# Kernel tuning notes

Measured on AMD Instinct MI355X. Metric: run time of the kernel, lower is better.

The kernel has to match this reference:

```python
import jax, jax.numpy as jnp
import numpy as np

B, T, D, H, P, A = 128, 512, 512, 512, 512, 32  # envs, steps, feat, lstm hidden, latent, actions


def setup_inputs() -> dict:
    key = jax.random.key(0)
    ks = jax.random.split(key, 30)
    N = B * T
    lin = lambda k, o, i: 0.02 * jax.random.normal(k, (o, i), jnp.float32)
    vec = lambda k, o: 0.02 * jax.random.normal(k, (o,), jnp.float32)
    inp = {
        'features': jax.random.normal(ks[0], (N, D), jnp.float32),
        'episode_starts': (jax.random.uniform(ks[1], (N,)) < 0.02).astype(jnp.float32),
        'h0_pi': jax.random.normal(ks[2], (1, B, H), jnp.float32),
        'c0_pi': jax.random.normal(ks[3], (1, B, H), jnp.float32),
        'h0_vf': jax.random.normal(ks[4], (1, B, H), jnp.float32),
        'c0_vf': jax.random.normal(ks[5], (1, B, H), jnp.float32),
        'Wih_pi': lin(ks[6], 4 * H, D), 'Whh_pi': lin(ks[7], 4 * H, H),
        'bih_pi': vec(ks[8], 4 * H), 'bhh_pi': vec(ks[9], 4 * H),
        'Wih_vf': lin(ks[10], 4 * H, D), 'Whh_vf': lin(ks[11], 4 * H, H),
        'bih_vf': vec(ks[12], 4 * H), 'bhh_vf': vec(ks[13], 4 * H),
        'pol_w1': lin(ks[14], P, H), 'pol_b1': vec(ks[15], P),
        'pol_w2': lin(ks[16], P, P), 'pol_b2': vec(ks[17], P),
        'val_w1': lin(ks[18], P, H), 'val_b1': vec(ks[19], P),
        'val_w2': lin(ks[20], P, P), 'val_b2': vec(ks[21], P),
        'actor_w': lin(ks[22], A, P), 'actor_b': vec(ks[23], A),
        'critic_w': lin(ks[24], 1, P), 'critic_b': vec(ks[25], 1),
        'deterministic': 1,
    }
    return inp


def masked_lstm(xs, starts, h0, c0, Wih, Whh, bih, bhh):
    # xs: [T,B,D], starts: [T,B]; PyTorch gate order i,f,g,o; reset h,c where episode starts.
    def step(carry, inp):
        h, c = carry
        x, s = inp
        m = (1.0 - s)[:, None]
        h, c = h * m, c * m
        g = x @ Wih.T + bih + h @ Whh.T + bhh
        i, f, gg, o = jnp.split(g, 4, axis=-1)
        c = jax.nn.sigmoid(f) * c + jax.nn.sigmoid(i) * jnp.tanh(gg)
        h = jax.nn.sigmoid(o) * jnp.tanh(c)
        return (h, c), h
    (hT, cT), ys = jax.lax.scan(step, (h0[0], c0[0]), (xs, starts))
    return ys, hT[None], cT[None]


def mlp(x, w1, b1, w2, b2):
    return jax.nn.relu(x @ w1.T + b1) @ w2.T + b2


def reference(features, episode_starts, h0_pi, c0_pi, h0_vf, c0_vf,
              Wih_pi, Whh_pi, bih_pi, bhh_pi, Wih_vf, Whh_vf, bih_vf, bhh_vf,
              pol_w1, pol_b1, pol_w2, pol_b2, val_w1, val_b1, val_w2, val_b2,
              actor_w, actor_b, critic_w, critic_b, deterministic):
    n_seq = h0_pi.shape[1]
    d = features.shape[-1]
    xs = features.reshape(n_seq, -1, d).swapaxes(0, 1)        # [T,B,D]
    st = episode_starts.reshape(n_seq, -1).swapaxes(0, 1)     # [T,B]
    ys_pi, h_pi, c_pi = masked_lstm(xs, st, h0_pi, c0_pi, Wih_pi, Whh_pi, bih_pi, bhh_pi)
    ys_vf, h_vf, c_vf = masked_lstm(xs, st, h0_vf, c0_vf, Wih_vf, Whh_vf, bih_vf, bhh_vf)
    hsz = ys_pi.shape[-1]
    lat_pi = ys_pi.swapaxes(0, 1).reshape(-1, hsz)            # [B*T,H]
    lat_vf = ys_vf.swapaxes(0, 1).reshape(-1, hsz)
    lat_pi = mlp(lat_pi, pol_w1, pol_b1, pol_w2, pol_b2)
    lat_vf = mlp(lat_vf, val_w1, val_b1, val_w2, val_b2)
    values = lat_vf @ critic_w.T + critic_b                    # [B*T,1]
    logits = lat_pi @ actor_w.T + actor_b                      # [B*T,A]
    actions = jnp.argmax(logits, axis=-1)                      # deterministic mode
    logp = jax.nn.log_softmax(logits, axis=-1)
    log_prob = jnp.take_along_axis(logp, actions[:, None], axis=1)[:, 0]
    return actions, values, log_prob, h_pi, c_pi, h_vf, c_vf
```

## Files before the change

### kernel.cpp

```cpp
#include <hip/hip_runtime.h>
#include <math.h>

#define BB 128
#define TT 512
#define DD 512
#define HH 512
#define NN (BB*TT)
#define PP 512
#define AA 32
#define CH 64
#define CR (BB*CH)

typedef unsigned short u16;
typedef unsigned int   u32;
typedef __attribute__((ext_vector_type(8))) short short8;
typedef __attribute__((ext_vector_type(4))) float f32x4;

__device__ __forceinline__ u16 f2bf(float f){
    u32 x = __float_as_uint(f);
    u32 r = (x + 0x7fffu + ((x >> 16) & 1u)) >> 16;
    return (u16)r;
}
__device__ __forceinline__ float bf2f(u16 u){
    return __uint_as_float(((u32)u) << 16);
}
__device__ __forceinline__ f32x4 mfma16(short8 a, short8 b, f32x4 c){
    return __builtin_amdgcn_mfma_f32_16x16x32_bf16(a, b, c, 0, 0, 0);
}
__device__ __forceinline__ float sigm(float x){
    return 1.f/(1.f + __expf(-x));
}
__device__ __forceinline__ float tanh_f(float x){
    return 1.f - 2.f/(1.f + __expf(2.f*x));
}

__global__ __launch_bounds__(256) void prep_lstm_w(
    const float* __restrict__ Wih_pi, const float* __restrict__ Whh_pi,
    const float* __restrict__ bih_pi, const float* __restrict__ bhh_pi,
    const float* __restrict__ Wih_vf, const float* __restrict__ Whh_vf,
    const float* __restrict__ bih_vf, const float* __restrict__ bhh_vf,
    u16* __restrict__ wihHi, u16* __restrict__ wihLo,
    u16* __restrict__ whhHi, u16* __restrict__ whhLo,
    float* __restrict__ biasP)
{
    long i = (long)blockIdx.x*256 + threadIdx.x;
    if (i >= 2L*2048*512) return;
    int L = (int)(i >> 20);
    int rem = (int)(i & 1048575);
    int c = rem >> 9, k = rem & 511;
    int u = c >> 2, g = c & 3;
    long src = (long)(g*512 + u)*512 + k;
    float wih = (L ? Wih_vf : Wih_pi)[src];
    float whh = (L ? Whh_vf : Whh_pi)[src];
    u16 h1 = f2bf(wih); wihHi[i] = h1; wihLo[i] = f2bf(wih - bf2f(h1));
    u16 h2 = f2bf(whh); whhHi[i] = h2; whhLo[i] = f2bf(whh - bf2f(h2));
    if (k == 0) {
        float b = (L ? bih_vf : bih_pi)[g*512+u] + (L ? bhh_vf : bhh_pi)[g*512+u];
        biasP[L*2048 + c] = b;
    }
}

__global__ __launch_bounds__(256) void prep_mlp_w(
    const float* __restrict__ w1pi, const float* __restrict__ w1vf,
    const float* __restrict__ w2pi, const float* __restrict__ w2vf,
    const float* __restrict__ b1pi, const float* __restrict__ b1vf,
    const float* __restrict__ b2pi, const float* __restrict__ b2vf,
    u16* __restrict__ mHi, u16* __restrict__ mLo, float* __restrict__ biasM)
{
    long i = (long)blockIdx.x*256 + threadIdx.x;
    if (i >= 4L*262144) return;
    int mat = (int)(i >> 18);
    int rem = (int)(i & 262143);
    const float* src = mat==0 ? w1pi : mat==1 ? w1vf : mat==2 ? w2pi : w2vf;
    float v = src[rem];
    u16 h = f2bf(v); mHi[i] = h; mLo[i] = f2bf(v - bf2f(h));
    if (rem < 512) {
        const float* bs = mat==0 ? b1pi : mat==1 ? b1vf : mat==2 ? b2pi : b2vf;
        biasM[mat*512 + rem] = bs[rem];
    }
}

__global__ __launch_bounds__(256) void init_state_k(
    const float* __restrict__ h0_pi, const float* __restrict__ c0_pi,
    const float* __restrict__ h0_vf, const float* __restrict__ c0_vf,
    const float* __restrict__ starts,
    u16* __restrict__ hHi, u16* __restrict__ hLo, float* __restrict__ cT,
    float* __restrict__ startsT)
{
    int i = blockIdx.x*256 + threadIdx.x;
    if (i < NN) {
        int e = i >> 9, t = i & 511;
        startsT[t*128 + e] = starts[i];
    }
    if (i >= 2*BB*HH) return;
    int L = i >> 16; int r = i & 65535;
    int e = r >> 9, u = r & 511;
    float m = 1.0f - starts[(long)e*TT];
    float h = (L ? h0_vf : h0_pi)[r] * m;
    float c = (L ? c0_vf : c0_pi)[r] * m;
    long hidx = (long)(L*2)*65536 + r;
    u16 hh = f2bf(h);
    hHi[hidx] = hh; hLo[hidx] = f2bf(h - bf2f(hh));
    cT[(long)L*65536 + (long)u*128 + e] = c;
}

template<int AM, int EM>
__global__ __launch_bounds__(256) void gemm_k512(
    const float* __restrict__ Afp,
    const u16* __restrict__ aHi, const u16* __restrict__ aLo, long aZ,
    int rowSh, int rowOuterHi, int rowOuterLo, int rowBase,
    const u16* __restrict__ bHi, const u16* __restrict__ bLo, long bZ,
    const float* __restrict__ bias, long biasZ,
    float* __restrict__ outF, long outFZ, int outLd,
    u16* __restrict__ oHi, u16* __restrict__ oLo, long oZ)
{
    __shared__ u16 sAh[5120], sAl[5120], sBh[5120], sBl[5120];
    const int tid = threadIdx.x;
    const int z = blockIdx.z;
    const long Mbase = (long)blockIdx.x * 128;
    const long Nbase = (long)blockIdx.y * 128;
    const int r2 = tid >> 1, half = tid & 1;
    const long mstage = Mbase + r2;
    const long arow = (mstage >> rowSh) * (long)rowOuterHi
                    + (mstage & (((long)1<<rowSh)-1)) * (long)rowOuterLo + rowBase;
    const long brow = Nbase + r2;
    const int wid = tid >> 6, lane = tid & 63;
    const int mh = wid & 1, nh = wid >> 1;
    const int l15 = lane & 15, quad = lane >> 4;

    f32x4 acc[4][4];
    #pragma unroll
    for (int i = 0; i < 4; ++i)
        #pragma unroll
        for (int j = 0; j < 4; ++j)
            acc[i][j] = (f32x4){0.f,0.f,0.f,0.f};

    const int sOffW = r2*40 + half*16;

    for (int kt = 0; kt < 16; ++kt) {
        const int k0 = kt*32;
        if constexpr (AM == 0) {
            const float* ap = Afp + arow*512 + k0 + half*16;
            float fv[16];
            #pragma unroll
            for (int q = 0; q < 4; ++q) *(float4*)(fv + q*4) = ((const float4*)ap)[q];
            short8 vh0, vh1, vl0, vl1;
            #pragma unroll
            for (int i = 0; i < 8; ++i){
                u16 h  = f2bf(fv[i]);   vh0[i] = (short)h;  vl0[i] = (short)f2bf(fv[i]   - bf2f(h));
                u16 h2 = f2bf(fv[8+i]); vh1[i] = (short)h2; vl1[i] = (short)f2bf(fv[8+i] - bf2f(h2));
            }
            *(short8*)(sAh + sOffW) = vh0; *(short8*)(sAh + sOffW + 8) = vh1;
            *(short8*)(sAl + sOffW) = vl0; *(short8*)(sAl + sOffW + 8) = vl1;
        } else {
            const u16* ph = aHi + (long)z*aZ + arow*512 + k0 + half*16;
            const u16* pl = aLo + (long)z*aZ + arow*512 + k0 + half*16;
            *(short8*)(sAh + sOffW) = *(const short8*)ph;
            *(short8*)(sAh + sOffW + 8) = *(const short8*)(ph + 8);
            *(short8*)(sAl + sOffW) = *(const short8*)pl;
            *(short8*)(sAl + sOffW + 8) = *(const short8*)(pl + 8);
        }
        {
            const u16* ph = bHi + (long)z*bZ + brow*512 + k0 + half*16;
            const u16* pl = bLo + (long)z*bZ + brow*512 + k0 + half*16;
            *(short8*)(sBh + sOffW) = *(const short8*)ph;
            *(short8*)(sBh + sOffW + 8) = *(const short8*)(ph + 8);
            *(short8*)(sBl + sOffW) = *(const short8*)pl;
            *(short8*)(sBl + sOffW + 8) = *(const short8*)(pl + 8);
        }
        __syncthreads();
        short8 bh[4], bl[4];
        #pragma unroll
        for (int nt = 0; nt < 4; ++nt){
            int bo = (nh*64 + nt*16 + l15)*40 + quad*8;
            bh[nt] = *(const short8*)(sBh + bo);
            bl[nt] = *(const short8*)(sBl + bo);
        }
        #pragma unroll
        for (int mt = 0; mt < 4; ++mt){
            int ao = (mh*64 + mt*16 + l15)*40 + quad*8;
            short8 ah = *(const short8*)(sAh + ao);
            short8 al = *(const short8*)(sAl + ao);
            #pragma unroll
            for (int nt = 0; nt < 4; ++nt){
                acc[mt][nt] = mfma16(ah, bh[nt], acc[mt][nt]);
                acc[mt][nt] = mfma16(ah, bl[nt], acc[mt][nt]);
                acc[mt][nt] = mfma16(al, bh[nt], acc[mt][nt]);
            }
        }
        __syncthreads();
    }
    #pragma unroll
    for (int nt = 0; nt < 4; ++nt){
        const long col = Nbase + nh*64 + nt*16 + l15;
        const float bv = bias[(long)z*biasZ + col];
        #pragma unroll
        for (int mt = 0; mt < 4; ++mt){
            const long rowm = Mbase + mh*64 + mt*16 + quad*4;
            #pragma unroll
            for (int rr = 0; rr < 4; ++rr){
                float v = acc[mt][nt][rr] + bv;
                const long m = rowm + rr;
                if constexpr (EM == 0) {
                    outF[(long)z*outFZ + m*(long)outLd + col] = v;
                } else {
                    if constexpr (EM == 1) v = fmaxf(v, 0.f);
                    u16 h = f2bf(v);
                    u16 l = f2bf(v - bf2f(h));
                    oHi[(long)z*oZ + m*512 + col] = h;
                    oLo[(long)z*oZ + m*512 + col] = l;
                }
            }
        }
    }
}

__global__ __launch_bounds__(256) void lstm_step2(
    u16* __restrict__ hHi, u16* __restrict__ hLo,
    const u16* __restrict__ whhHi, const u16* __restrict__ whhLo,
    const float* __restrict__ gx,
    const float* __restrict__ startsT,
    float* __restrict__ cT,
    u16* __restrict__ ysHi, u16* __restrict__ ysLo,
    float* __restrict__ dout, int t, int tau)
{
    __shared__ __attribute__((aligned(16))) u16 sA[2][16384];
    __shared__ float zsm[4][144];

    const int tid  = threadIdx.x;
    const int wc   = blockIdx.x;
    const int eb   = blockIdx.y;
    const int L    = blockIdx.z;
    const int wid  = tid >> 6, lane = tid & 63;
    const int l15  = lane & 15, quad = lane >> 4;
    const int p    = t & 1;
    const int ebase = eb*64;
    const int e    = ebase + wid*16 + l15;

    {
        const size_t wbase = (size_t)L*1048576 + (size_t)(wc*32)*512;
        #pragma unroll
        for (int i = 0; i < 16; ++i){
            int f = tid + i*256;
            int pl = f >> 11;
            int r2 = f & 2047;
            int wcol = r2 >> 6, ksg = r2 & 63;
            const u16* src = (pl ? whhLo : whhHi) + wbase + (size_t)wcol*512 + ksg*8;
            int dst = (ksg>>2)*1024 + wcol*32 + (ksg&3)*8;
            *(short8*)(sA[pl] + dst) = *(const short8*)src;
        }
    }
    __syncthreads();

    const u16* hHiP = hHi + (size_t)((L*2+p)*128 + e)*512 + quad*8;
    const u16* hLoP = hLo + (size_t)((L*2+p)*128 + e)*512 + quad*8;

    f32x4 acc0 = (f32x4){0.f,0.f,0.f,0.f};
    f32x4 acc1 = (f32x4){0.f,0.f,0.f,0.f};
    #pragma unroll
    for (int kt = 0; kt < 16; ++kt){
        short8 bh = *(const short8*)(hHiP + kt*32);
        short8 bl = *(const short8*)(hLoP + kt*32);
        int a0 = kt*1024 + l15*32 + quad*8;
        short8 ah0 = *(const short8*)(sA[0] + a0);
        short8 al0 = *(const short8*)(sA[1] + a0);
        short8 ah1 = *(const short8*)(sA[0] + a0 + 512);
        short8 al1 = *(const short8*)(sA[1] + a0 + 512);
        acc0 = mfma16(ah0, bh, acc0);
        acc0 = mfma16(ah0, bl, acc0);
        acc0 = mfma16(al0, bh, acc0);
        acc1 = mfma16(ah1, bh, acc1);
        acc1 = mfma16(ah1, bl, acc1);
        acc1 = mfma16(al1, bh, acc1);
    }

    const float mn = (t < TT-1) ? (1.0f - startsT[(t+1)*128 + e]) : 1.0f;
    const size_t gxrow = ((size_t)L*CR + (size_t)tau*128 + e)*2048 + wc*32;
    #pragma unroll
    for (int mt = 0; mt < 2; ++mt){
        const int u = wc*8 + mt*4 + quad;
        float4 gv = *(const float4*)(gx + gxrow + mt*16 + quad*4);
        f32x4 z = mt ? acc1 : acc0;
        float ii = sigm(z[0] + gv.x);
        float ff = sigm(z[1] + gv.y);
        float gg = tanh_f(z[2] + gv.z);
        float oo = sigm(z[3] + gv.w);
        size_t ci = (size_t)L*65536 + (size_t)u*128 + e;
        float cn = ff*cT[ci] + ii*gg;
        float hn = oo * tanh_f(cn);
        cT[ci] = cn * mn;
        zsm[wid][l15*8 + mt*4 + quad] = hn;
        if (mt == 0) zsm[wid][128 + l15] = mn;
        if (t == TT-1) {
            dout[(size_t)(3+2*L)*NN + (size_t)e*512 + u] = hn;
            dout[(size_t)(4+2*L)*NN + (size_t)e*512 + u] = cn;
        }
    }
    __syncthreads();

    {
        const int role = quad;
        const int e2 = l15;
        const int eg = ebase + wid*16 + e2;
        float v[8];
        #pragma unroll
        for (int j = 0; j < 8; ++j) v[j] = zsm[wid][e2*8 + j];
        const float mn2 = zsm[wid][128 + e2];
        short8 pk;
        if (role < 2) {
            #pragma unroll
            for (int j = 0; j < 8; ++j){
                float hm = v[j] * mn2;
                u16 h = f2bf(hm);
                pk[j] = (short)(role == 0 ? h : f2bf(hm - bf2f(h)));
            }
            u16* dst = (role == 0 ? hHi : hLo)
                     + (size_t)((L*2 + (1-p))*128 + eg)*512 + wc*8;
            *(short8*)dst = pk;
        } else {
            #pragma unroll
            for (int j = 0; j < 8; ++j){
                u16 h = f2bf(v[j]);
                pk[j] = (short)(role == 2 ? h : f2bf(v[j] - bf2f(h)));
            }
            u16* dst = (role == 2 ? ysHi : ysLo)
                     + ((size_t)L*CR + (size_t)tau*128 + eg)*512 + wc*8;
            *(short8*)dst = pk;
        }
    }
}

__global__ __launch_bounds__(256) void head_pi(
    const u16* __restrict__ latHi, const u16* __restrict__ latLo,
    const float* __restrict__ actor_w, const float* __restrict__ actor_b,
    float* __restrict__ dout, int t0)
{
    __shared__ float latS[16*516];
    __shared__ float lg[16*36];
    const int tid = threadIdx.x;
    const long r0 = (long)blockIdx.x * 16;
    {
        int rr = tid >> 4, seg = tid & 15;
        const u16* ph = latHi + (r0 + rr)*512 + seg*32;
        const u16* pl = latLo + (r0 + rr)*512 + seg*32;
        float* dst = latS + rr*516 + seg*32;
        #pragma unroll
        for (int ii = 0; ii < 4; ++ii){
            short8 vh = *(const short8*)(ph + ii*8);
            short8 vl = *(const short8*)(pl + ii*8);
            #pragma unroll
            for (int jj = 0; jj < 8; ++jj)
                dst[ii*8+jj] = bf2f((u16)vh[jj]) + bf2f((u16)vl[jj]);
        }
    }
    __syncthreads();
    {
        int rr = tid >> 4, a0 = (tid & 15)*2;
        const float4* lrow = (const float4*)(latS + rr*516);
        float acc0 = actor_b[a0], acc1 = actor_b[a0+1];
        for (int kq = 0; kq < 128; ++kq){
            float4 lv = lrow[kq];
            float4 w0 = ((const float4*)actor_w)[(a0  )*128 + kq];
            float4 w1 = ((const float4*)actor_w)[(a0+1)*128 + kq];
            acc0 += lv.x*w0.x + lv.y*w0.y + lv.z*w0.z + lv.w*w0.w;
            acc1 += lv.x*w1.x + lv.y*w1.y + lv.z*w1.z + lv.w*w1.w;
        }
        lg[rr*36 + a0]   = acc0;
        lg[rr*36 + a0+1] = acc1;
    }
    __syncthreads();
    if (tid < 16){
        float mx = -INFINITY; int am = 0;
        #pragma unroll
        for (int a = 0; a < AA; ++a){
            float v = lg[tid*36 + a];
            if (v > mx){ mx = v; am = a; }
        }
        float se = 0.f;
        #pragma unroll
        for (int a = 0; a < AA; ++a) se += expf(lg[tid*36 + a] - mx);
        long row = r0 + tid;
        long n = (row & 127)*TT + t0 + (row >> 7);
        dout[n] = (float)am;
        dout[2L*NN + n] = -logf(se);
    }
}

__global__ __launch_bounds__(256) void head_vf(
    const u16* __restrict__ latHi, const u16* __restrict__ latLo,
    const float* __restrict__ critic_w, const float* __restrict__ critic_b,
    float* __restrict__ dout, int t0)
{
    __shared__ float part[256];
    const int tid = threadIdx.x;
    const long r0 = (long)blockIdx.x * 32;
    int rr = tid >> 3, seg = tid & 7;
    const u16* ph = latHi + (r0 + rr)*512 + seg*64;
    const u16* pl = latLo + (r0 + rr)*512 + seg*64;
    float acc = 0.f;
    #pragma unroll
    for (int ii = 0; ii < 8; ++ii){
        short8 vh = *(const short8*)(ph + ii*8);
        short8 vl = *(const short8*)(pl + ii*8);
        #pragma unroll
        for (int jj = 0; jj < 8; ++jj){
            float lv = bf2f((u16)vh[jj]) + bf2f((u16)vl[jj]);
            acc += lv * critic_w[seg*64 + ii*8 + jj];
        }
    }
    part[tid] = acc;
    __syncthreads();
    if (tid < 32){
        float v = critic_b[0];
        #pragma unroll
        for (int s = 0; s < 8; ++s) v += part[tid*8 + s];
        long row = r0 + tid;
        long n = (row & 127)*TT + t0 + (row >> 7);
        dout[(long)NN + n] = v;
    }
}

extern "C" void kernel_launch(void* const* d_in, const int* in_sizes, int n_in,
                              void* d_out, int out_size, void* d_ws, size_t ws_size,
                              hipStream_t stream) {
    const float* features = (const float*)d_in[0];
    const float* starts   = (const float*)d_in[1];
    const float* h0_pi = (const float*)d_in[2];
    const float* c0_pi = (const float*)d_in[3];
    const float* h0_vf = (const float*)d_in[4];
    const float* c0_vf = (const float*)d_in[5];
    const float* Wih_pi = (const float*)d_in[6];
    const float* Whh_pi = (const float*)d_in[7];
    const float* bih_pi = (const float*)d_in[8];
    const float* bhh_pi = (const float*)d_in[9];
    const float* Wih_vf = (const float*)d_in[10];
    const float* Whh_vf = (const float*)d_in[11];
    const float* bih_vf = (const float*)d_in[12];
    const float* bhh_vf = (const float*)d_in[13];
    const float* pol_w1 = (const float*)d_in[14];
    const float* pol_b1 = (const float*)d_in[15];
    const float* pol_w2 = (const float*)d_in[16];
    const float* pol_b2 = (const float*)d_in[17];
    const float* val_w1 = (const float*)d_in[18];
    const float* val_b1 = (const float*)d_in[19];
    const float* val_w2 = (const float*)d_in[20];
    const float* val_b2 = (const float*)d_in[21];
    const float* actor_w  = (const float*)d_in[22];
    const float* actor_b  = (const float*)d_in[23];
    const float* critic_w = (const float*)d_in[24];
    const float* critic_b = (const float*)d_in[25];
    float* out = (float*)d_out;

    size_t off = 0;
    auto alloc = [&](size_t b) {
        void* p = (char*)d_ws + off;
        off += (b + 255) & ~(size_t)255;
        return p;
    };
    u16* wihHi = (u16*)alloc(2L*2048*512*2);
    u16* wihLo = (u16*)alloc(2L*2048*512*2);
    u16* whhHi = (u16*)alloc(2L*2048*512*2);
    u16* whhLo = (u16*)alloc(2L*2048*512*2);
    float* biasP = (float*)alloc(2L*2048*4);
    u16* mHi = (u16*)alloc(4L*262144*2);
    u16* mLo = (u16*)alloc(4L*262144*2);
    float* biasM = (float*)alloc(4L*512*4);
    u16* hHi = (u16*)alloc(2L*2*128*512*2);
    u16* hLo = (u16*)alloc(2L*2*128*512*2);
    float* cT  = (float*)alloc(2L*128*512*4);
    float* startsT = (float*)alloc((size_t)NN*4);
    u16* ysHi = (u16*)alloc(2L*CR*512*2);
    u16* ysLo = (u16*)alloc(2L*CR*512*2);
    u16* hidHi = (u16*)alloc(2L*CR*512*2);
    u16* hidLo = (u16*)alloc(2L*CR*512*2);
    u16* latHi = (u16*)alloc(2L*CR*512*2);
    u16* latLo = (u16*)alloc(2L*CR*512*2);
    float* gxF = (float*)alloc(2L*CR*2048*4);
    const long gxZ = (long)CR*2048;
    const long pZ  = (long)CR*512;

    prep_lstm_w<<<dim3(8192), dim3(256), 0, stream>>>(
        Wih_pi, Whh_pi, bih_pi, bhh_pi, Wih_vf, Whh_vf, bih_vf, bhh_vf,
        wihHi, wihLo, whhHi, whhLo, biasP);
    prep_mlp_w<<<dim3(4096), dim3(256), 0, stream>>>(
        pol_w1, val_w1, pol_w2, val_w2, pol_b1, val_b1, pol_b2, val_b2,
        mHi, mLo, biasM);
    init_state_k<<<dim3(512), dim3(256), 0, stream>>>(
        h0_pi, c0_pi, h0_vf, c0_vf, starts, hHi, hLo, cT, startsT);

    for (int t0 = 0; t0 < TT; t0 += CH) {
        gemm_k512<0,0><<<dim3(CR/128, 16, 2), dim3(256), 0, stream>>>(
            features, nullptr, nullptr, 0L,
            7, 1, 512, t0,
            wihHi, wihLo, 1048576L,
            biasP, 2048L,
            gxF, gxZ, 2048,
            nullptr, nullptr, 0L);
        for (int tau = 0; tau < CH; ++tau) {
            lstm_step2<<<dim3(64, 2, 2), dim3(256), 0, stream>>>(
                hHi, hLo, whhHi, whhLo, gxF, startsT, cT, ysHi, ysLo,
                out, t0 + tau, tau);
        }
        gemm_k512<1,1><<<dim3(CR/128, 4, 2), dim3(256), 0, stream>>>(
            nullptr, ysHi, ysLo, pZ,
            30, 0, 1, 0,
            mHi, mLo, 262144L,
            biasM, 512L,
            nullptr, 0L, 0,
            hidHi, hidLo, pZ);
        gemm_k512<1,2><<<dim3(CR/128, 4, 2), dim3(256), 0, stream>>>(
            nullptr, hidHi, hidLo, pZ,
            30, 0, 1, 0,
            mHi + 2L*262144, mLo + 2L*262144, 262144L,
            biasM + 1024, 512L,
            nullptr, 0L, 0,
            latHi, latLo, pZ);
        head_pi<<<dim3(CR/16), dim3(256), 0, stream>>>(
            latHi, latLo, actor_w, actor_b, out, t0);
        head_vf<<<dim3(CR/32), dim3(256), 0, stream>>>(
            latHi + pZ, latLo + pZ, critic_w, critic_b, out, t0);
    }
}
```

Before: 7.455 ms.

## Make LSTM chunk persistent with grid barriers instead of per-step launches

Replaces the 64 per-timestep LSTM kernel launches per chunk with one persistent kernel that loops over the chunk's timesteps. Blocks synchronise through an atomic-counter grid barrier, using one counter per step, which init_state_k zeroes. The recurrent weights stay in LDS and the cell state stays in registers across steps. This removes launch overhead and the repeated weight reloads, but it requires all 256 blocks to be co-resident and adds spin-wait barrier latency.

```diff
diff --git a/kernel.cpp b/kernel.cpp
--- a/kernel.cpp
+++ b/kernel.cpp
@@ -32,6 +32,18 @@
 }
 __device__ __forceinline__ float tanh_f(float x){
     return 1.f - 2.f/(1.f + __expf(2.f*x));
+}
+
+__device__ __forceinline__ void grid_barrier(unsigned* bar, unsigned nblk){
+    __syncthreads();
+    if (threadIdx.x == 0){
+        __threadfence();
+        __hip_atomic_fetch_add(bar, 1u, __ATOMIC_ACQ_REL, __HIP_MEMORY_SCOPE_AGENT);
+        while (__hip_atomic_load(bar, __ATOMIC_ACQUIRE, __HIP_MEMORY_SCOPE_AGENT) < nblk)
+            __builtin_amdgcn_s_sleep(1);
+    }
+    __syncthreads();
+    __threadfence();
 }
 
 __global__ __launch_bounds__(256) void prep_lstm_w(
@@ -85,9 +97,10 @@
     const float* __restrict__ h0_vf, const float* __restrict__ c0_vf,
     const float* __restrict__ starts,
     u16* __restrict__ hHi, u16* __restrict__ hLo, float* __restrict__ cT,
-    float* __restrict__ startsT)
+    float* __restrict__ startsT, unsigned* __restrict__ bar)
 {
     int i = blockIdx.x*256 + threadIdx.x;
+    if (i < 512) bar[i] = 0u;
     if (i < NN) {
         int e = i >> 9, t = i & 511;
         startsT[t*128 + e] = starts[i];
@@ -215,14 +228,14 @@
     }
 }
 
-__global__ __launch_bounds__(256) void lstm_step2(
+__global__ __launch_bounds__(256) void lstm_chunk(
     u16* __restrict__ hHi, u16* __restrict__ hLo,
     const u16* __restrict__ whhHi, const u16* __restrict__ whhLo,
     const float* __restrict__ gx,
     const float* __restrict__ startsT,
     float* __restrict__ cT,
     u16* __restrict__ ysHi, u16* __restrict__ ysLo,
-    float* __restrict__ dout, int t, int tau)
+    float* __restrict__ dout, unsigned* __restrict__ bar, int t0)
 {
     __shared__ __attribute__((aligned(16))) u16 sA[2][16384];
     __shared__ float zsm[4][144];
@@ -233,7 +246,6 @@
     const int L    = blockIdx.z;
     const int wid  = tid >> 6, lane = tid & 63;
     const int l15  = lane & 15, quad = lane >> 4;
-    const int p    = t & 1;
     const int ebase = eb*64;
     const int e    = ebase + wid*16 + l15;
 
@@ -252,82 +264,113 @@
     }
     __syncthreads();
 
-    const u16* hHiP = hHi + (size_t)((L*2+p)*128 + e)*512 + quad*8;
-    const u16* hLoP = hLo + (size_t)((L*2+p)*128 + e)*512 + quad*8;
-
-    f32x4 acc0 = (f32x4){0.f,0.f,0.f,0.f};
-    f32x4 acc1 = (f32x4){0.f,0.f,0.f,0.f};
-    #pragma unroll
-    for (int kt = 0; kt < 16; ++kt){
-        short8 bh = *(const short8*)(hHiP + kt*32);
-        short8 bl = *(const short8*)(hLoP + kt*32);
-        int a0 = kt*1024 + l15*32 + quad*8;
-        short8 ah0 = *(const short8*)(sA[0] + a0);
-        short8 al0 = *(const short8*)(sA[1] + a0);
-        short8 ah1 = *(const short8*)(sA[0] + a0 + 512);
-        short8 al1 = *(const short8*)(sA[1] + a0 + 512);
-        acc0 = mfma16(ah0, bh, acc0);
-        acc0 = mfma16(ah0, bl, acc0);
-        acc0 = mfma16(al0, bh, acc0);
-        acc1 = mfma16(ah1, bh, acc1);
-        acc1 = mfma16(ah1, bl, acc1);
-        acc1 = mfma16(al1, bh, acc1);
-    }
-
-    const float mn = (t < TT-1) ? (1.0f - startsT[(t+1)*128 + e]) : 1.0f;
-    const size_t gxrow = ((size_t)L*CR + (size_t)tau*128 + e)*2048 + wc*32;
-    #pragma unroll
-    for (int mt = 0; mt < 2; ++mt){
-        const int u = wc*8 + mt*4 + quad;
-        float4 gv = *(const float4*)(gx + gxrow + mt*16 + quad*4);
-        f32x4 z = mt ? acc1 : acc0;
-        float ii = sigm(z[0] + gv.x);
-        float ff = sigm(z[1] + gv.y);
-        float gg = tanh_f(z[2] + gv.z);
-        float oo = sigm(z[3] + gv.w);
-        size_t ci = (size_t)L*65536 + (size_t)u*128 + e;
-        float cn = ff*cT[ci] + ii*gg;
-        float hn = oo * tanh_f(cn);
-        cT[ci] = cn * mn;
-        zsm[wid][l15*8 + mt*4 + quad] = hn;
-        if (mt == 0) zsm[wid][128 + l15] = mn;
-        if (t == TT-1) {
-            dout[(size_t)(3+2*L)*NN + (size_t)e*512 + u] = hn;
-            dout[(size_t)(4+2*L)*NN + (size_t)e*512 + u] = cn;
-        }
-    }
-    __syncthreads();
-
-    {
-        const int role = quad;
-        const int e2 = l15;
-        const int eg = ebase + wid*16 + e2;
-        float v[8];
-        #pragma unroll
-        for (int j = 0; j < 8; ++j) v[j] = zsm[wid][e2*8 + j];
-        const float mn2 = zsm[wid][128 + e2];
-        short8 pk;
-        if (role < 2) {
+    const int u0 = wc*8 + quad;
+    const int u1 = wc*8 + 4 + quad;
+    const size_t ci0 = (size_t)L*65536 + (size_t)u0*128 + e;
+    const size_t ci1 = (size_t)L*65536 + (size_t)u1*128 + e;
+    float c0 = cT[ci0];
+    float c1 = cT[ci1];
+
+    const size_t hrowOff = (size_t)e*512 + quad*8;
+    const size_t gxbase  = ((size_t)L*CR + e)*2048 + wc*32 + quad*4;
+
+    for (int tau = 0; tau < CH; ++tau){
+        const int t = t0 + tau;
+        const int p = t & 1;
+
+        const float* gp = gx + gxbase + (size_t)tau*(128*2048);
+        float4 gv0 = *(const float4*)(gp);
+        float4 gv1 = *(const float4*)(gp + 16);
+        const float mn = (t < TT-1) ? (1.0f - startsT[(t+1)*128 + e]) : 1.0f;
+
+        const u16* hHiP = hHi + (size_t)(L*2+p)*65536 + hrowOff;
+        const u16* hLoP = hLo + (size_t)(L*2+p)*65536 + hrowOff;
+        f32x4 acc0 = (f32x4){0.f,0.f,0.f,0.f};
+        f32x4 acc1 = (f32x4){0.f,0.f,0.f,0.f};
+        #pragma unroll
+        for (int kt = 0; kt < 16; ++kt){
+            short8 bh = *(const short8*)(hHiP + kt*32);
+            short8 bl = *(const short8*)(hLoP + kt*32);
+            int a0 = kt*1024 + l15*32 + quad*8;
+            short8 ah0 = *(const short8*)(sA[0] + a0);
+            short8 al0 = *(const short8*)(sA[1] + a0);
+            short8 ah1 = *(const short8*)(sA[0] + a0 + 512);
+            short8 al1 = *(const short8*)(sA[1] + a0 + 512);
+            acc0 = mfma16(ah0, bh, acc0);
+            acc0 = mfma16(ah0, bl, acc0);
+            acc0 = mfma16(al0, bh, acc0);
+            acc1 = mfma16(ah1, bh, acc1);
+            acc1 = mfma16(ah1, bl, acc1);
+            acc1 = mfma16(al1, bh, acc1);
+        }
+
+        {
+            float ii = sigm(acc0[0] + gv0.x);
+            float ff = sigm(acc0[1] + gv0.y);
+            float gg = tanh_f(acc0[2] + gv0.z);
+            float oo = sigm(acc0[3] + gv0.w);
+            float cn = ff*c0 + ii*gg;
+            float hn = oo * tanh_f(cn);
+            c0 = cn * mn;
+            zsm[wid][l15*8 + quad] = hn;
+            zsm[wid][128 + l15] = mn;
+            if (t == TT-1) {
+                dout[(size_t)(3+2*L)*NN + (size_t)e*512 + u0] = hn;
+                dout[(size_t)(4+2*L)*NN + (size_t)e*512 + u0] = cn;
+            }
+        }
+        {
+            float ii = sigm(acc1[0] + gv1.x);
+            float ff = sigm(acc1[1] + gv1.y);
+            float gg = tanh_f(acc1[2] + gv1.z);
+            float oo = sigm(acc1[3] + gv1.w);
+            float cn = ff*c1 + ii*gg;
+            float hn = oo * tanh_f(cn);
+            c1 = cn * mn;
+            zsm[wid][l15*8 + 4 + quad] = hn;
+            if (t == TT-1) {
+                dout[(size_t)(3+2*L)*NN + (size_t)e*512 + u1] = hn;
+                dout[(size_t)(4+2*L)*NN + (size_t)e*512 + u1] = cn;
+            }
+        }
+        __syncthreads();
+
+        {
+            const int role = quad;
+            const int e2 = l15;
+            const int eg = ebase + wid*16 + e2;
+            float v[8];
             #pragma unroll
-            for (int j = 0; j < 8; ++j){
-                float hm = v[j] * mn2;
-                u16 h = f2bf(hm);
-                pk[j] = (short)(role == 0 ? h : f2bf(hm - bf2f(h)));
+            for (int j = 0; j < 8; ++j) v[j] = zsm[wid][e2*8 + j];
+            const float mn2 = zsm[wid][128 + e2];
+            short8 pk;
+            if (role < 2) {
+                #pragma unroll
+                for (int j = 0; j < 8; ++j){
+                    float hm = v[j] * mn2;
+                    u16 h = f2bf(hm);
+                    pk[j] = (short)(role == 0 ? h : f2bf(hm - bf2f(h)));
+                }
+                u16* dst = (role == 0 ? hHi : hLo)
+                         + (size_t)(L*2 + (1-p))*65536 + (size_t)eg*512 + wc*8;
+                *(short8*)dst = pk;
+            } else {
+                #pragma unroll
+                for (int j = 0; j < 8; ++j){
+                    u16 h = f2bf(v[j]);
+                    pk[j] = (short)(role == 2 ? h : f2bf(v[j] - bf2f(h)));
+                }
+                u16* dst = (role == 2 ? ysHi : ysLo)
+                         + ((size_t)L*CR + (size_t)tau*128 + eg)*512 + wc*8;
+                *(short8*)dst = pk;
             }
-            u16* dst = (role == 0 ? hHi : hLo)
-                     + (size_t)((L*2 + (1-p))*128 + eg)*512 + wc*8;
-            *(short8*)dst = pk;
-        } else {
-            #pragma unroll
-            for (int j = 0; j < 8; ++j){
-                u16 h = f2bf(v[j]);
-                pk[j] = (short)(role == 2 ? h : f2bf(v[j] - bf2f(h)));
-            }
-            u16* dst = (role == 2 ? ysHi : ysLo)
-                     + ((size_t)L*CR + (size_t)tau*128 + eg)*512 + wc*8;
-            *(short8*)dst = pk;
-        }
-    }
+        }
+
+        if (tau < CH-1) grid_barrier(bar + t0 + tau, 256u);
+    }
+
+    cT[ci0] = c0;
+    cT[ci1] = c1;
 }
 
 __global__ __launch_bounds__(256) void head_pi(
@@ -469,6 +512,7 @@
     u16* hLo = (u16*)alloc(2L*2*128*512*2);
     float* cT  = (float*)alloc(2L*128*512*4);
     float* startsT = (float*)alloc((size_t)NN*4);
+    unsigned* bar = (unsigned*)alloc(512*4);
     u16* ysHi = (u16*)alloc(2L*CR*512*2);
     u16* ysLo = (u16*)alloc(2L*CR*512*2);
     u16* hidHi = (u16*)alloc(2L*CR*512*2);
@@ -486,7 +530,7 @@
         pol_w1, val_w1, pol_w2, val_w2, pol_b1, val_b1, pol_b2, val_b2,
         mHi, mLo, biasM);
     init_state_k<<<dim3(512), dim3(256), 0, stream>>>(
-        h0_pi, c0_pi, h0_vf, c0_vf, starts, hHi, hLo, cT, startsT);
+        h0_pi, c0_pi, h0_vf, c0_vf, starts, hHi, hLo, cT, startsT, bar);
 
     for (int t0 = 0; t0 < TT; t0 += CH) {
         gemm_k512<0,0><<<dim3(CR/128, 16, 2), dim3(256), 0, stream>>>(
@@ -496,11 +540,9 @@
             biasP, 2048L,
             gxF, gxZ, 2048,
             nullptr, nullptr, 0L);
-        for (int tau = 0; tau < CH; ++tau) {
-            lstm_step2<<<dim3(64, 2, 2), dim3(256), 0, stream>>>(
-                hHi, hLo, whhHi, whhLo, gxF, startsT, cT, ysHi, ysLo,
-                out, t0 + tau, tau);
-        }
+        lstm_chunk<<<dim3(64, 2, 2), dim3(256), 0, stream>>>(
+            hHi, hLo, whhHi, whhLo, gxF, startsT, cT, ysHi, ysLo,
+            out, bar, t0);
         gemm_k512<1,1><<<dim3(CR/128, 4, 2), dim3(256), 0, stream>>>(
             nullptr, ysHi, ysLo, pZ,
             30, 0, 1, 0,
```

After: 27.56 ms. 3.7x slower.
